# Performance work log

Hardware: AMD Instinct MI355X
Metric: run time of the kernel (lower is better)

Reference implementation:

```python
import jax, jax.numpy as jnp
import numpy as np

B = 2
L = 512                         # latent dim
NF = [64, 128, 256, 512, 512]   # _get_num_features(2*base_features=64, 64, max=512)


def _rn(key, shape, scale=1.0):
    return scale * jax.random.normal(key, shape, dtype=jnp.float32)


def _blur_up(x):
    """upfirdn2d: 2x upsample + FIR blur with resample_kernel [1,3,3,1], gain=factor**2."""
    k = jnp.array([1.0, 3.0, 3.0, 1.0], dtype=x.dtype)
    kk = jnp.outer(k, k)
    kk = kk / kk.sum() * 4.0  # gain = 2**2
    c = x.shape[-1]
    kern = jnp.broadcast_to(kk[:, :, None, None], (4, 4, 1, c))
    return jax.lax.conv_general_dilated(
        x, kern, (1, 1), ((2, 2), (2, 2)), lhs_dilation=(2, 2),
        dimension_numbers=('NHWC', 'HWIO', 'NHWC'), feature_group_count=c)


def _mod_conv(x, latent, w, b, sw, sb, demodulate):
    """StyleGAN2 modulated conv. x:(B,H,W,Cin), w:(kh,kw,Cin,Cout), style affine (L,Cin)."""
    s = latent @ sw + sb                             # (B,Cin) style
    ww = w[None] * s[:, None, None, :, None]         # (B,kh,kw,Cin,Cout)
    if demodulate:
        d = jax.lax.rsqrt(jnp.sum(ww * ww, axis=(1, 2, 3)) + 1e-8)  # (B,Cout)
        ww = ww * d[:, None, None, None, :]
    def per_sample(xi, wi):
        return jax.lax.conv_general_dilated(
            xi[None], wi, (1, 1), 'SAME',
            dimension_numbers=('NHWC', 'HWIO', 'NHWC'))[0]
    return jax.vmap(per_sample)(x, ww) + b


def _forward(latents, const, w0, b0, sw0, sb0, ns0, noise0, wr0, br0, swr0, sbr0,
             wu1, bu1, swu1, sbu1, wc1, bc1, swc1, sbc1, wr1, br1, swr1, sbr1,
             wu2, bu2, swu2, sbu2, wc2, bc2, swc2, sbc2, wr2, br2, swr2, sbr2,
             wu3, bu3, swu3, sbu3, wc3, bc3, swc3, sbc3, wr3, br3, swr3, sbr3,
             wu4, bu4, swu4, sbu4, wc4, bc4, swc4, sbc4, wr4, br4, swr4, sbr4):
    act = lambda t: jax.nn.leaky_relu(t, 0.01)
    b = latents.shape[0]
    lat = latents.reshape(b, 2, 5, latents.shape[-1])  # (B,2,n_levels,L)
    # first layer at 4x4: modulated conv + noise + leaky_relu (only layer with noise, per source)
    y = _mod_conv(jnp.tile(const[None], (b, 1, 1, 1)), lat[:, 0, 0], w0, b0, sw0, sb0, True)
    y = act(y + ns0 * noise0)
    rgb = act(_mod_conv(y, lat[:, 0, 1], wr0, br0, swr0, sbr0, False))
    ups = [(wu1, bu1, swu1, sbu1), (wu2, bu2, swu2, sbu2), (wu3, bu3, swu3, sbu3), (wu4, bu4, swu4, sbu4)]
    cvs = [(wc1, bc1, swc1, sbc1), (wc2, bc2, swc2, sbc2), (wc3, bc3, swc3, sbc3), (wc4, bc4, swc4, sbc4)]
    rgbs = [(wr1, br1, swr1, sbr1), (wr2, br2, swr2, sbr2), (wr3, br3, swr3, sbr3), (wr4, br4, swr4, sbr4)]
    for i in range(1, 5):
        wu, bu, swu, sbu = ups[i - 1]
        wc, bc, swc, sbc = cvs[i - 1]
        wr, br, swr, sbr = rgbs[i - 1]
        y = _mod_conv(_blur_up(y), lat[:, i - 1, 1], wu, bu, swu, sbu, True)
        # plain ModulatedConv2D 3x3 (no noise/activation in the source loop)
        y = _mod_conv(y, lat[:, i, 0], wc, bc, swc, sbc, True)
        # to_rgb (no demod) + skip accumulation of FIR-upsampled previous rgb
        rgb = act(_mod_conv(y, lat[:, i, 1], wr, br, swr, sbr, False)) + _blur_up(rgb)
    return rgb  # (B,64,64,3)


reference = _forward


def setup_inputs():
    key = jax.random.key(0)
    ks = iter(jax.random.split(key, 80))
    inp = {}
    inp['latents'] = _rn(next(ks), (B, 2 * 5, L))
    inp['const'] = _rn(next(ks), (4, 4, NF[-1]))
    def mod(pfx, kh, cin, cout):
        inp['w' + pfx] = _rn(next(ks), (kh, kh, cin, cout), (kh * kh * cin) ** -0.5)
        inp['b' + pfx] = jnp.zeros((cout,), jnp.float32)
        inp['sw' + pfx] = _rn(next(ks), (L, cin), L ** -0.5)
        inp['sb' + pfx] = jnp.ones((cin,), jnp.float32)
    mod('0', 3, NF[-1], NF[-1])
    inp['ns0'] = 0.1 * _rn(next(ks), (1, 1, 1, 1))
    inp['noise0'] = _rn(next(ks), (B, 4, 4, 1))
    mod('r0', 1, NF[-1], 3)
    cprev = NF[-1]
    for i in range(1, 5):
        c = NF[i]
        mod('u%d' % i, 3, cprev, c)
        mod('c%d' % i, 3, c, c)
        mod('r%d' % i, 1, c, 3)
        cprev = c
    return inp
```

## Files before the change

kernel.cpp:

```cpp
#include <hip/hip_runtime.h>

#define LEAKY(v) ((v) > 0.f ? (v) : 0.01f * (v))

typedef __attribute__((ext_vector_type(8))) short bf16x8;
typedef __attribute__((ext_vector_type(4))) short bf16x4;
typedef __attribute__((ext_vector_type(4))) float floatx4;

__device__ inline unsigned short f2bf(float f) {
  unsigned u = __float_as_uint(f);
  unsigned r = u + 0x7FFFu + ((u >> 16) & 1u);
  return (unsigned short)(r >> 16);
}

__device__ inline bf16x8 ld_frag8(const unsigned short* p) {
  bf16x4 lo = *(const bf16x4*)p;
  bf16x4 hi = *(const bf16x4*)(p + 4);
  return __builtin_shufflevector(lo, hi, 0, 1, 2, 3, 4, 5, 6, 7);
}

struct StyleDesc { const float* sw; const float* sb; int row; int cin; };
struct StyleArgs { StyleDesc d[14]; };
struct W2D { const float* w; int cinLog; int coutLog; int start; int w2off; };
struct W2Args { W2D d[9]; int total4; };
struct WTD { const float* src; unsigned short* dst; int cinLog; int coutLog; int start; };
struct WTArgs { WTD d[6]; int totalTiles; };

__device__ void style_body(int bid, const float* __restrict__ lat, const StyleArgs& A,
                           float* __restrict__ S)
{
  int chunk = bid & 1, b = (bid >> 1) & 1, sid = bid >> 2;
  StyleDesc d = A.d[sid];
  int ci = chunk * 256 + threadIdx.x;
  if (ci >= d.cin) return;
  const float* l = lat + (size_t)b * (10 * 512) + d.row * 512;
  float a0 = 0.f, a1 = 0.f, a2 = 0.f, a3 = 0.f, a4 = 0.f, a5 = 0.f, a6 = 0.f, a7 = 0.f;
  const float* wp = d.sw + ci;
  size_t st = d.cin;
  for (int k = 0; k < 512; k += 8) {
    a0 += l[k] * wp[0];
    a1 += l[k + 1] * wp[st];
    a2 += l[k + 2] * wp[2 * st];
    a3 += l[k + 3] * wp[3 * st];
    a4 += l[k + 4] * wp[4 * st];
    a5 += l[k + 5] * wp[5 * st];
    a6 += l[k + 6] * wp[6 * st];
    a7 += l[k + 7] * wp[7 * st];
    wp += 8 * st;
  }
  S[sid * 1024 + b * 512 + ci] = d.sb[ci] + ((a0 + a1) + (a2 + a3)) + ((a4 + a5) + (a6 + a7));
}

__device__ void w2_body(int idx, const W2Args& A, float* __restrict__ W2)
{
  if (idx >= A.total4) return;
  int c = 0;
  while (c < 8 && idx >= A.d[c + 1].start) c++;
  W2D d = A.d[c];
  int rel = idx - d.start;
  int co4Log = d.coutLog - 2;
  int ci = rel >> co4Log;
  int co = (rel & ((1 << co4Log) - 1)) << 2;
  size_t ktStride = (size_t)(1 << d.cinLog) << d.coutLog;
  const float* p = d.w + ((size_t)ci << d.coutLog) + co;
  float4 acc = {0.f, 0.f, 0.f, 0.f};
#pragma unroll
  for (int kt = 0; kt < 9; kt++) {
    float4 v = *(const float4*)(p + kt * ktStride);
    acc.x += v.x * v.x; acc.y += v.y * v.y; acc.z += v.z * v.z; acc.w += v.w * v.w;
  }
  *(float4*)(W2 + d.w2off + ((size_t)ci << d.coutLog) + co) = acc;
}

__device__ void wprep_tile_body(int tile, const WTArgs& A, unsigned short* __restrict__ tl)
{
  int c = 0;
  while (c < 5 && tile >= A.d[c + 1].start) c++;
  WTD d = A.d[c];
  int rel = tile - d.start;
  int coTiles = 1 << (d.coutLog - 6);
  int cig = rel / coTiles;
  int co0 = (rel - cig * coTiles) << 6;
  int cin = 1 << d.cinLog, cout = 1 << d.coutLog;
  int tid = threadIdx.x;
  for (int slot = tid; slot < 288 * 16; slot += 256) {
    int r = slot >> 4;
    int co4 = slot & 15;
    int kt = r >> 5, cisub = r & 31;
    const float* sp = d.src + ((size_t)(kt * cin + (cig << 5) + cisub) << d.coutLog) + co0 + co4 * 4;
    float4 v = *(const float4*)sp;
    int cb = co4 * 4;
    tl[(cb + 0) * 296 + r] = f2bf(v.x);
    tl[(cb + 1) * 296 + r] = f2bf(v.y);
    tl[(cb + 2) * 296 + r] = f2bf(v.z);
    tl[(cb + 3) * 296 + r] = f2bf(v.w);
  }
  __syncthreads();
  int Kp = cin * 9;
  for (int slot = tid; slot < 64 * 36; slot += 256) {
    int co = slot / 36, c8 = slot - (slot / 36) * 36;
    bf16x4 lo = *(const bf16x4*)(tl + co * 296 + c8 * 8);
    bf16x4 hi = *(const bf16x4*)(tl + co * 296 + c8 * 8 + 4);
    unsigned short* op = d.dst + (size_t)(co0 + co) * Kp + cig * 288 + c8 * 8;
    *(bf16x4*)op = lo;
    *(bf16x4*)(op + 4) = hi;
  }
}

__global__ __launch_bounds__(256) void prep_all_kernel(
    const float* __restrict__ lat, StyleArgs SA, W2Args WA, WTArgs TA,
    float* __restrict__ S, float* __restrict__ W2, int styleBlocks, int w2Blocks)
{
  __shared__ unsigned short tl[64 * 296];
  int bid = blockIdx.x;
  if (bid < styleBlocks) { style_body(bid, lat, SA, S); return; }
  bid -= styleBlocks;
  if (bid < w2Blocks) { w2_body(bid * 256 + threadIdx.x, WA, W2); return; }
  bid -= w2Blocks;
  if (bid < TA.totalTiles) wprep_tile_body(bid, TA, tl);
}

struct D2D { int w2off; int sid; int did; int cin; int cout; int start; };
struct D2Args { D2D d[9]; };

__global__ __launch_bounds__(256) void demod2_all_kernel(
    D2Args A, const float* __restrict__ W2, const float* __restrict__ S,
    float* __restrict__ Dout)
{
  __shared__ float red[256];
  int bid = blockIdx.x;
  int c = 0;
  while (c < 8 && bid >= A.d[c + 1].start) c++;
  D2D d = A.d[c];
  int rel = bid - d.start;
  int chunksPerB = d.cout >> 6;
  int b = rel / chunksPerB;
  int coc = rel - b * chunksPerB;
  int co = coc * 64 + (threadIdx.x & 63);
  int slice = threadIdx.x >> 6;
  const float* sv = S + d.sid * 1024 + b * 512;
  const float* wp = W2 + d.w2off + co;
  float a0 = 0.f, a1 = 0.f, a2 = 0.f, a3 = 0.f, a4 = 0.f, a5 = 0.f, a6 = 0.f, a7 = 0.f;
  for (int r = slice; r < d.cin; r += 32) {
    float s0 = sv[r];          a0 += s0 * s0 * wp[(size_t)r * d.cout];
    float s1 = sv[r + 4];      a1 += s1 * s1 * wp[(size_t)(r + 4) * d.cout];
    float s2 = sv[r + 8];      a2 += s2 * s2 * wp[(size_t)(r + 8) * d.cout];
    float s3 = sv[r + 12];     a3 += s3 * s3 * wp[(size_t)(r + 12) * d.cout];
    float s4 = sv[r + 16];     a4 += s4 * s4 * wp[(size_t)(r + 16) * d.cout];
    float s5 = sv[r + 20];     a5 += s5 * s5 * wp[(size_t)(r + 20) * d.cout];
    float s6 = sv[r + 24];     a6 += s6 * s6 * wp[(size_t)(r + 24) * d.cout];
    float s7 = sv[r + 28];     a7 += s7 * s7 * wp[(size_t)(r + 28) * d.cout];
  }
  red[threadIdx.x] = ((a0 + a1) + (a2 + a3)) + ((a4 + a5) + (a6 + a7));
  __syncthreads();
  if (threadIdx.x < 64) {
    float a = red[threadIdx.x] + red[threadIdx.x + 64] + red[threadIdx.x + 128] + red[threadIdx.x + 192];
    Dout[d.did * 1024 + b * 512 + co] = rsqrtf(a + 1e-8f);
  }
}

__device__ inline void blur_taps(int o, int* r0, int* r1, float* w0, float* w1)
{
  if ((o & 1) == 0) { *r0 = (o >> 1) - 1; *w0 = 1.f; *r1 = (o >> 1); *w1 = 3.f; }
  else              { *r0 = (o - 1) >> 1; *w0 = 3.f; *r1 = ((o - 1) >> 1) + 1; *w1 = 1.f; }
}

__global__ __launch_bounds__(256) void prep_up_kernel(
    const float* __restrict__ y, int Hc, int C,
    const float* __restrict__ s, unsigned short* __restrict__ out)
{
  int b = blockIdx.y;
  int W2 = Hc * 2;
  int pix = blockIdx.x;
  int oy = pix / W2, ox = pix - oy * W2;
  int ry0, ry1, rx0, rx1; float wy0, wy1, wx0, wx1;
  blur_taps(oy, &ry0, &ry1, &wy0, &wy1);
  blur_taps(ox, &rx0, &rx1, &wx0, &wx1);
  bool vy0 = (ry0 >= 0 && ry0 < Hc), vy1 = (ry1 >= 0 && ry1 < Hc);
  bool vx0 = (rx0 >= 0 && rx0 < Hc), vx1 = (rx1 >= 0 && rx1 < Hc);
  const float* base = y + (size_t)b * Hc * Hc * C;
  unsigned short* ob = out + (((size_t)b * W2 + oy) * W2 + ox) * C;
  const float* sv = s + b * 512;
  for (int c = threadIdx.x; c < C; c += 256) {
    float acc = 0.f;
    if (vy0) {
      const float* r = base + (size_t)(ry0 * Hc) * C;
      if (vx0) acc += wy0 * wx0 * r[(size_t)rx0 * C + c];
      if (vx1) acc += wy0 * wx1 * r[(size_t)rx1 * C + c];
    }
    if (vy1) {
      const float* r = base + (size_t)(ry1 * Hc) * C;
      if (vx0) acc += wy1 * wx0 * r[(size_t)rx0 * C + c];
      if (vx1) acc += wy1 * wx1 * r[(size_t)rx1 * C + c];
    }
    ob[c] = f2bf(acc * (1.f / 16.f) * sv[c]);
  }
}

__global__ __launch_bounds__(256) void mfma_conv_kernel(
    const unsigned short* __restrict__ xp, int H, int WLOG, int Cin, int Cout,
    const unsigned short* __restrict__ wT,
    const float* __restrict__ bias, const float* __restrict__ dmod,
    float* __restrict__ outF, unsigned short* __restrict__ outBf,
    const float* __restrict__ sNext)
{
  extern __shared__ unsigned short sm[];
  const int W = 1 << WLOG;
  const int Rt = 128 >> WLOG;
  const int PR = Rt + 2, PC = W + 2;
  const int patchU = PR * PC * 36;
  unsigned short* Bw = sm + patchU;

  const int tid = threadIdx.x;
  const int wave = tid >> 6;
  const int lane = tid & 63;
  const int q = lane >> 4;
  const int l15 = lane & 15;

  const int HW = H << WLOG;
  const int m0 = blockIdx.x << 7;
  const int b = m0 / HW;
  const int y0 = (m0 - b * HW) >> WLOG;
  const int co0 = blockIdx.y << 6;
  const int Kp = Cin * 9;
  const unsigned short* xb = xp + (size_t)b * HW * Cin;

  const int pSlots = PR * PC * 4;
  int pLds[5], pSrc[5];
#pragma unroll
  for (int i = 0; i < 5; i++) {
    int sidx = tid + i * 256;
    pLds[i] = -1; pSrc[i] = -1;
    if (sidx < pSlots) {
      int pidx = sidx >> 2, part = sidx & 3;
      int pr = pidx / PC, pc = pidx - pr * PC;
      int gy = y0 + pr - 1, gx = pc - 1;
      pLds[i] = pidx * 36 + part * 8;
      if ((unsigned)gy < (unsigned)H && (unsigned)gx < (unsigned)W)
        pSrc[i] = ((gy << WLOG) + gx) * Cin + part * 8;
    }
  }
  int bLds[9], bSrc[9];
#pragma unroll
  for (int i = 0; i < 9; i++) {
    int sidx = tid + i * 256;
    int n = sidx / 36, c16 = sidx - n * 36;
    bLds[i] = n * 292 + c16 * 8;
    bSrc[i] = (co0 + n) * Kp + c16 * 8;
  }

  floatx4 zero = {0.f, 0.f, 0.f, 0.f};
  floatx4 acc[2][4];
#pragma unroll
  for (int mi = 0; mi < 2; mi++)
#pragma unroll
    for (int s = 0; s < 4; s++) acc[mi][s] = zero;

  const int mA0 = wave * 32 + l15;
  const int mA1 = mA0 + 16;
  const int aBase0 = ((mA0 >> WLOG) * PC + (mA0 & (W - 1))) * 36 + q * 8;
  const int aBase1 = ((mA1 >> WLOG) * PC + (mA1 & (W - 1))) * 36 + q * 8;
  const int bBase = l15 * 292 + q * 8;

  const int nGroups = Cin >> 5;

  uint4 pv[5], bv[9];
  {
#pragma unroll
    for (int i = 0; i < 5; i++) {
      uint4 v = {0u, 0u, 0u, 0u};
      if (pLds[i] >= 0 && pSrc[i] >= 0) v = *(const uint4*)(xb + pSrc[i]);
      pv[i] = v;
    }
#pragma unroll
    for (int i = 0; i < 9; i++) bv[i] = *(const uint4*)(wT + bSrc[i]);
  }

  for (int g = 0; g < nGroups; g++) {
    __syncthreads();
#pragma unroll
    for (int i = 0; i < 5; i++) {
      if (pLds[i] >= 0) {
        uint2 lo = {pv[i].x, pv[i].y}, hi = {pv[i].z, pv[i].w};
        *(uint2*)(sm + pLds[i]) = lo;
        *(uint2*)(sm + pLds[i] + 4) = hi;
      }
    }
#pragma unroll
    for (int i = 0; i < 9; i++) {
      uint2 lo = {bv[i].x, bv[i].y}, hi = {bv[i].z, bv[i].w};
      *(uint2*)(Bw + bLds[i]) = lo;
      *(uint2*)(Bw + bLds[i] + 4) = hi;
    }
    __syncthreads();
    if (g + 1 < nGroups) {
      const int gci = (g + 1) << 5;
      const int gw = (g + 1) * 288;
#pragma unroll
      for (int i = 0; i < 5; i++) {
        uint4 v = {0u, 0u, 0u, 0u};
        if (pLds[i] >= 0 && pSrc[i] >= 0) v = *(const uint4*)(xb + pSrc[i] + gci);
        pv[i] = v;
      }
#pragma unroll
      for (int i = 0; i < 9; i++) bv[i] = *(const uint4*)(wT + bSrc[i] + gw);
    }
#pragma unroll
    for (int kt = 0; kt < 9; kt++) {
      const int ky = kt / 3, kx = kt - (kt / 3) * 3;
      const int ao = (ky * PC + kx) * 36;
      bf16x8 a0 = ld_frag8(sm + aBase0 + ao);
      bf16x8 a1 = ld_frag8(sm + aBase1 + ao);
      const int bo = bBase + kt * 32;
#pragma unroll
      for (int s = 0; s < 4; s++) {
        bf16x8 bb = ld_frag8(Bw + bo + s * (16 * 292));
        acc[0][s] = __builtin_amdgcn_mfma_f32_16x16x32_bf16(a0, bb, acc[0][s], 0, 0, 0);
        acc[1][s] = __builtin_amdgcn_mfma_f32_16x16x32_bf16(a1, bb, acc[1][s], 0, 0, 0);
      }
    }
  }

#pragma unroll
  for (int s = 0; s < 4; s++) {
    const int co = co0 + s * 16 + l15;
    const float dm = dmod[b * 512 + co];
    const float bv2 = bias[co];
    const float sn = sNext ? sNext[b * 512 + co] : 0.f;
#pragma unroll
    for (int mi = 0; mi < 2; mi++) {
#pragma unroll
      for (int r = 0; r < 4; r++) {
        const int mloc = wave * 32 + mi * 16 + q * 4 + r;
        const int py = y0 + (mloc >> WLOG);
        const int px = mloc & (W - 1);
        const size_t oidx = (((size_t)b * H + py) * W + px) * Cout + co;
        const float v = acc[mi][s][r] * dm + bv2;
        if (outF) outF[oidx] = v;
        if (outBf) outBf[oidx] = f2bf(v * sn);
      }
    }
  }
}

template<int PIX, int NCI4>
__global__ __launch_bounds__(256) void modconv_splitk_kernel(
    const float* __restrict__ x, size_t xBStride, int H, int W, int cinShift,
    int Cout,
    const float* __restrict__ w, const float* __restrict__ s,
    float* __restrict__ partial)
{
  constexpr int NCI = NCI4 * 4;
  constexpr int CLOG = (NCI == 16) ? 4 : (NCI == 32) ? 5 : 6;
  extern __shared__ float lds[];
  const int COLS = PIX + 2;
  const int tid = threadIdx.x;
  const int nthr = blockDim.x;
  const int b = blockIdx.y;
  const int z = blockIdx.z;
  const int ci0 = z << CLOG;
  const int wb = W / PIX;
  const int row = blockIdx.x / wb;
  const int x0 = (blockIdx.x % wb) * PIX;

  const float* xb = x + (size_t)b * xBStride;
  const float* sv = s + b * 512;

  const int tot = 3 * COLS << CLOG;
  for (int idx = tid; idx < tot; idx += nthr) {
    int cil = idx & (NCI - 1);
    int t = idx >> CLOG;
    int col = t % COLS;
    int ry = t / COLS;
    int gy = row + ry - 1;
    int gx = x0 + col - 1;
    float v = 0.f;
    if (gy >= 0 && gy < H && gx >= 0 && gx < W)
      v = xb[((size_t)(gy * W + gx) << cinShift) + ci0 + cil] * sv[ci0 + cil];
    lds[idx] = v;
  }
  __syncthreads();

  float acc0[PIX];
  float acc1[PIX];
#pragma unroll
  for (int p = 0; p < PIX; p++) { acc0[p] = 0.f; acc1[p] = 0.f; }
  const int co0 = tid;
  const int co1 = tid + nthr;
  const bool a0 = co0 < Cout;
  const bool a1 = co1 < Cout;
  const int d01 = nthr;

  const float4* ldsv = (const float4*)lds;
  constexpr int cin4Shift = CLOG - 2;

  for (int kt = 0; kt < 9; kt++) {
    int ky = kt / 3, kx = kt % 3;
    const float* wr = w + ((size_t)(kt << cinShift) + ci0) * Cout + co0;
#pragma unroll
    for (int c4 = 0; c4 < NCI4; c4++) {
      float wA0 = 0.f, wA1 = 0.f, wA2 = 0.f, wA3 = 0.f;
      float wB0 = 0.f, wB1 = 0.f, wB2 = 0.f, wB3 = 0.f;
      const float* wq = wr + (size_t)c4 * 4 * Cout;
      if (a0) { wA0 = wq[0]; }
      if (a1) { wB0 = wq[d01]; }
      if (a0) { wA1 = wq[Cout]; }
      if (a1) { wB1 = wq[Cout + d01]; }
      if (a0) { wA2 = wq[2 * Cout]; }
      if (a1) { wB2 = wq[2 * Cout + d01]; }
      if (a0) { wA3 = wq[3 * Cout]; }
      if (a1) { wB3 = wq[3 * Cout + d01]; }
#pragma unroll
      for (int p = 0; p < PIX; p++) {
        float4 v = ldsv[((ky * COLS + kx + p) << cin4Shift) + c4];
        acc0[p] += v.x * wA0; acc0[p] += v.y * wA1; acc0[p] += v.z * wA2; acc0[p] += v.w * wA3;
        acc1[p] += v.x * wB0; acc1[p] += v.y * wB1; acc1[p] += v.z * wB2; acc1[p] += v.w * wB3;
      }
    }
  }

  const int HW = H * W;
  float* pb = partial + ((size_t)(z * gridDim.y + b) * HW + row * W + x0) * Cout;
#pragma unroll
  for (int p = 0; p < PIX; p++) {
    if (a0) pb[(size_t)p * Cout + co0] = acc0[p];
    if (a1) pb[(size_t)p * Cout + co1] = acc1[p];
  }
}

__global__ __launch_bounds__(128) void modconv_splitk_blur_kernel(
    const float* __restrict__ y, const float* __restrict__ w,
    const float* __restrict__ s, float* __restrict__ partial)
{
  extern __shared__ float lds[];
  const int tid = threadIdx.x;
  const int b = blockIdx.y;
  const int z = blockIdx.z;
  const int ci0 = z << 4;
  const int row = blockIdx.x;

  const float* yb = y + (size_t)b * 16 * 512;
  const float* sv = s + b * 512;

  for (int idx = tid; idx < 480; idx += 128) {
    int cil = idx & 15;
    int t = idx >> 4;
    int col = t % 10;
    int ry = t / 10;
    int gy = row + ry - 1;
    int gx = col - 1;
    float v = 0.f;
    if ((unsigned)gy < 8u && (unsigned)gx < 8u) {
      int ry0, ry1, rx0, rx1; float wy0, wy1, wx0, wx1;
      blur_taps(gy, &ry0, &ry1, &wy0, &wy1);
      blur_taps(gx, &rx0, &rx1, &wx0, &wx1);
      bool vy0 = (ry0 >= 0 && ry0 < 4), vy1 = (ry1 >= 0 && ry1 < 4);
      bool vx0 = (rx0 >= 0 && rx0 < 4), vx1 = (rx1 >= 0 && rx1 < 4);
      int ci = ci0 + cil;
      float acc = 0.f;
      if (vy0 && vx0) acc += wy0 * wx0 * yb[((ry0 * 4 + rx0) << 9) + ci];
      if (vy0 && vx1) acc += wy0 * wx1 * yb[((ry0 * 4 + rx1) << 9) + ci];
      if (vy1 && vx0) acc += wy1 * wx0 * yb[((ry1 * 4 + rx0) << 9) + ci];
      if (vy1 && vx1) acc += wy1 * wx1 * yb[((ry1 * 4 + rx1) << 9) + ci];
      v = acc * (1.f / 16.f) * sv[ci];
    }
    lds[idx] = v;
  }
  __syncthreads();

  float acc0[8];
#pragma unroll
  for (int p = 0; p < 8; p++) acc0[p] = 0.f;
  const int co0 = tid;
  const float4* ldsv = (const float4*)lds;

  for (int kt = 0; kt < 9; kt++) {
    int ky = kt / 3, kx = kt % 3;
    const float* wr = w + ((size_t)(kt << 9) + ci0) * 128 + co0;
#pragma unroll
    for (int c4 = 0; c4 < 4; c4++) {
      const float* wq = wr + (size_t)c4 * 4 * 128;
      float wA0 = wq[0];
      float wA1 = wq[128];
      float wA2 = wq[256];
      float wA3 = wq[384];
#pragma unroll
      for (int p = 0; p < 8; p++) {
        float4 v = ldsv[((ky * 10 + kx + p) << 2) + c4];
        acc0[p] += v.x * wA0; acc0[p] += v.y * wA1; acc0[p] += v.z * wA2; acc0[p] += v.w * wA3;
      }
    }
  }

  float* pb = partial + ((size_t)(z * gridDim.y + b) * 64 + row * 8) * 128;
#pragma unroll
  for (int p = 0; p < 8; p++) pb[(size_t)p * 128 + co0] = acc0[p];
}

__global__ __launch_bounds__(256) void splitk_epi_kernel(
    const float* __restrict__ partial, int nz, int M, int Cout, int HW,
    const float* __restrict__ dmod, const float* __restrict__ bias,
    float* __restrict__ out)
{
  int idx = blockIdx.x * 256 + threadIdx.x;
  if (idx >= M * Cout) return;
  int m = idx / Cout;
  int co = idx - m * Cout;
  int b = m / HW;
  float acc = 0.f;
  for (int z = 0; z < nz; z++) acc += partial[(size_t)z * M * Cout + idx];
  out[idx] = acc * dmod[b * 512 + co] + bias[co];
}

__global__ void epirgb_kernel(
    const float* __restrict__ P, int nz, int HW, int Cout, int W,
    const float* __restrict__ dmod, const float* __restrict__ bias,
    const float* __restrict__ noise, const float* __restrict__ ns, int doAct,
    const float* __restrict__ sR, const float* __restrict__ wR, const float* __restrict__ bR,
    const float* __restrict__ prev,
    float* __restrict__ yout, float* __restrict__ rgbout)
{
  __shared__ float red[24];
  int b = blockIdx.x / HW;
  int pix = blockIdx.x - b * HW;
  int co = threadIdx.x;
  int m = b * HW + pix;
  float acc = 0.f;
  for (int z = 0; z < nz; z++) acc += P[((size_t)(z * 2 + b) * HW + pix) * Cout + co];
  float v = acc * dmod[b * 512 + co] + bias[co];
  if (noise) v += ns[0] * noise[m];
  if (doAct) v = LEAKY(v);
  yout[(size_t)m * Cout + co] = v;
  float t = v * sR[b * 512 + co];
  float r0 = t * wR[co * 3 + 0];
  float r1 = t * wR[co * 3 + 1];
  float r2 = t * wR[co * 3 + 2];
  for (int off = 32; off > 0; off >>= 1) {
    r0 += __shfl_down(r0, off);
    r1 += __shfl_down(r1, off);
    r2 += __shfl_down(r2, off);
  }
  int wv = threadIdx.x >> 6, lane = threadIdx.x & 63;
  if (lane == 0) { red[wv * 3 + 0] = r0; red[wv * 3 + 1] = r1; red[wv * 3 + 2] = r2; }
  __syncthreads();
  if (threadIdx.x == 0) {
    int nw = blockDim.x >> 6;
    float s0 = bR[0], s1 = bR[1], s2 = bR[2];
    for (int w = 0; w < nw; w++) { s0 += red[w * 3]; s1 += red[w * 3 + 1]; s2 += red[w * 3 + 2]; }
    s0 = LEAKY(s0); s1 = LEAKY(s1); s2 = LEAKY(s2);
    if (prev) {
      int oy = pix / W, ox = pix - (pix / W) * W;
      int Hp = W >> 1;
      int ry0, ry1, rx0, rx1; float wy0, wy1, wx0, wx1;
      blur_taps(oy, &ry0, &ry1, &wy0, &wy1);
      blur_taps(ox, &rx0, &rx1, &wx0, &wx1);
      bool vy0 = (ry0 >= 0 && ry0 < Hp), vy1 = (ry1 >= 0 && ry1 < Hp);
      bool vx0 = (rx0 >= 0 && rx0 < Hp), vx1 = (rx1 >= 0 && rx1 < Hp);
      const float* base = prev + (size_t)b * Hp * Hp * 3;
      float a0 = 0.f, a1 = 0.f, a2 = 0.f;
      if (vy0 && vx0) { const float* qq = base + (size_t)(ry0 * Hp + rx0) * 3; float wg = wy0 * wx0; a0 += wg * qq[0]; a1 += wg * qq[1]; a2 += wg * qq[2]; }
      if (vy0 && vx1) { const float* qq = base + (size_t)(ry0 * Hp + rx1) * 3; float wg = wy0 * wx1; a0 += wg * qq[0]; a1 += wg * qq[1]; a2 += wg * qq[2]; }
      if (vy1 && vx0) { const float* qq = base + (size_t)(ry1 * Hp + rx0) * 3; float wg = wy1 * wx0; a0 += wg * qq[0]; a1 += wg * qq[1]; a2 += wg * qq[2]; }
      if (vy1 && vx1) { const float* qq = base + (size_t)(ry1 * Hp + rx1) * 3; float wg = wy1 * wx1; a0 += wg * qq[0]; a1 += wg * qq[1]; a2 += wg * qq[2]; }
      s0 += a0 * (1.f / 16.f); s1 += a1 * (1.f / 16.f); s2 += a2 * (1.f / 16.f);
    }
    rgbout[(size_t)m * 3 + 0] = s0;
    rgbout[(size_t)m * 3 + 1] = s1;
    rgbout[(size_t)m * 3 + 2] = s2;
  }
}

__global__ __launch_bounds__(64) void rgb_kernel(
    const float* __restrict__ y, int H, int W, int Cin,
    const float* __restrict__ w, const float* __restrict__ bias,
    const float* __restrict__ s, const float* __restrict__ prev,
    float* __restrict__ out)
{
  int b = blockIdx.y;
  int pix = blockIdx.x;
  int oy = pix / W, ox = pix % W;
  const float* xp = y + (((size_t)b * H + oy) * W + ox) * Cin;
  const float* sv = s + b * 512;
  float p0 = 0.f, p1 = 0.f, p2 = 0.f;
  for (int ci = threadIdx.x; ci < Cin; ci += 64) {
    float v = xp[ci] * sv[ci];
    p0 += v * w[ci * 3 + 0];
    p1 += v * w[ci * 3 + 1];
    p2 += v * w[ci * 3 + 2];
  }
  for (int off = 32; off > 0; off >>= 1) {
    p0 += __shfl_down(p0, off);
    p1 += __shfl_down(p1, off);
    p2 += __shfl_down(p2, off);
  }
  if (threadIdx.x == 0) {
    float r0 = p0 + bias[0], r1 = p1 + bias[1], r2 = p2 + bias[2];
    float sk0 = 0.f, sk1 = 0.f, sk2 = 0.f;
    if (prev) {
      int Hp = H >> 1, Wp = W >> 1;
      int ry0, ry1, rx0, rx1; float wy0, wy1, wx0, wx1;
      blur_taps(oy, &ry0, &ry1, &wy0, &wy1);
      blur_taps(ox, &rx0, &rx1, &wx0, &wx1);
      bool vy0 = (ry0 >= 0 && ry0 < Hp), vy1 = (ry1 >= 0 && ry1 < Hp);
      bool vx0 = (rx0 >= 0 && rx0 < Wp), vx1 = (rx1 >= 0 && rx1 < Wp);
      const float* base = prev + (size_t)b * Hp * Wp * 3;
      float a0 = 0.f, a1 = 0.f, a2 = 0.f;
      if (vy0 && vx0) { const float* qq = base + (size_t)(ry0 * Wp + rx0) * 3; float wg = wy0 * wx0; a0 += wg * qq[0]; a1 += wg * qq[1]; a2 += wg * qq[2]; }
      if (vy0 && vx1) { const float* qq = base + (size_t)(ry0 * Wp + rx1) * 3; float wg = wy0 * wx1; a0 += wg * qq[0]; a1 += wg * qq[1]; a2 += wg * qq[2]; }
      if (vy1 && vx0) { const float* qq = base + (size_t)(ry1 * Wp + rx0) * 3; float wg = wy1 * wx0; a0 += wg * qq[0]; a1 += wg * qq[1]; a2 += wg * qq[2]; }
      if (vy1 && vx1) { const float* qq = base + (size_t)(ry1 * Wp + rx1) * 3; float wg = wy1 * wx1; a0 += wg * qq[0]; a1 += wg * qq[1]; a2 += wg * qq[2]; }
      sk0 = a0 * (1.f / 16.f); sk1 = a1 * (1.f / 16.f); sk2 = a2 * (1.f / 16.f);
    }
    float* ob = out + (((size_t)b * H + oy) * W + ox) * 3;
    ob[0] = LEAKY(r0) + sk0;
    ob[1] = LEAKY(r1) + sk1;
    ob[2] = LEAKY(r2) + sk2;
  }
}

extern "C" void kernel_launch(void* const* d_in, const int* in_sizes, int n_in,
                              void* d_out, int out_size, void* d_ws, size_t ws_size,
                              hipStream_t stream)
{
  auto F = [&](int k) { return (const float*)d_in[k]; };
  const float* latents = F(0);
  const float* cnst = F(1);
  const float* w0 = F(2);  const float* b0 = F(3);  const float* sw0 = F(4);  const float* sb0 = F(5);
  const float* ns0 = F(6); const float* noise0 = F(7);
  const float* wr0 = F(8); const float* br0 = F(9); const float* swr0 = F(10); const float* sbr0 = F(11);
  const float *wu[4], *bu[4], *swu[4], *sbu[4];
  const float *wc[4], *bc[4], *swc[4], *sbc[4];
  const float *wr[4], *br_[4], *swr[4], *sbr[4];
  int k = 12;
  for (int l = 0; l < 4; l++) {
    wu[l] = F(k++); bu[l] = F(k++); swu[l] = F(k++); sbu[l] = F(k++);
    wc[l] = F(k++); bc[l] = F(k++); swc[l] = F(k++); sbc[l] = F(k++);
    wr[l] = F(k++); br_[l] = F(k++); swr[l] = F(k++); sbr[l] = F(k++);
  }

  float* ws = (float*)d_ws;
  float* S = ws;
  float* D = S + 14 * 1024;
  float* W2 = D + 9 * 1024;
  float* bufA = W2 + 1359872;
  float* bufB = bufA + 2 * 64 * 64 * 512;
  float* rgbA = bufB + 2 * 64 * 64 * 512;
  float* rgbB = rgbA + 2 * 64 * 64 * 3;
  float* P = rgbB + 2 * 64 * 64 * 3;
  unsigned short* u16 = (unsigned short*)(P + 524288);
  unsigned short* xprepA = u16;
  unsigned short* xprepB = xprepA + 2 * 64 * 64 * 512;
  unsigned short* wT[6];
  {
    unsigned short* p = xprepB + 2 * 64 * 64 * 512;
    int wsz[6] = {9 * 128 * 256, 9 * 256 * 256, 9 * 256 * 512, 9 * 512 * 512, 9 * 512 * 512, 9 * 512 * 512};
    for (int i = 0; i < 6; i++) { wT[i] = p; p += wsz[i]; }
  }

  const int B = 2;
  const int NFa[5] = {64, 128, 256, 512, 512};
  int cprev0[4] = {512, 128, 256, 512};
  int rowu[4] = {1, 6, 6, 6};

  const float* cw[9]  = {w0, wu[0], wc[0], wu[1], wc[1], wu[2], wc[2], wu[3], wc[3]};
  int cinL[9]  = {9, 9, 7, 7, 8, 8, 9, 9, 9};
  int coutL[9] = {9, 7, 7, 8, 8, 9, 9, 9, 9};
  int sidOf[9] = {0, 2, 3, 5, 6, 8, 9, 11, 12};
  int didOf[9] = {0, 1, 2, 3, 4, 5, 6, 7, 8};

  int w2off[9];
  {
    StyleArgs SA;
    SA.d[0] = {sw0, sb0, 0, 512};
    SA.d[1] = {swr0, sbr0, 1, 512};
    for (int l = 0; l < 4; l++) {
      int c = NFa[l + 1];
      SA.d[2 + l * 3] = {swu[l], sbu[l], rowu[l], cprev0[l]};
      SA.d[3 + l * 3] = {swc[l], sbc[l], 5, c};
      SA.d[4 + l * 3] = {swr[l], sbr[l], 6, c};
    }
    W2Args WA2;
    int w2start = 0, off = 0;
    for (int i = 0; i < 9; i++) {
      w2off[i] = off;
      WA2.d[i] = {cw[i], cinL[i], coutL[i], w2start, off};
      int elems = 1 << (cinL[i] + coutL[i]);
      w2start += elems >> 2;
      off += elems;
    }
    WA2.total4 = w2start;
    WTArgs TA;
    {
      const float* srcs[6] = {wu[1], wc[1], wu[2], wc[2], wu[3], wc[3]};
      int cinLg[6] = {7, 8, 8, 9, 9, 9};
      int coutLg[6] = {8, 8, 9, 9, 9, 9};
      int start = 0;
      for (int i = 0; i < 6; i++) {
        TA.d[i] = {srcs[i], wT[i], cinLg[i], coutLg[i], start};
        start += (1 << (cinLg[i] - 5)) * (1 << (coutLg[i] - 6));
      }
      TA.totalTiles = start;
    }
    int styleBlocks = 56;
    int w2Blocks = (WA2.total4 + 255) / 256;
    prep_all_kernel<<<dim3(styleBlocks + w2Blocks + TA.totalTiles), 256, 0, stream>>>(
        latents, SA, WA2, TA, S, W2, styleBlocks, w2Blocks);
  }

  {
    D2Args DA;
    int start = 0;
    for (int i = 0; i < 9; i++) {
      int cout = 1 << coutL[i];
      DA.d[i] = {w2off[i], sidOf[i], didOf[i], 1 << cinL[i], cout, start};
      start += B * (cout >> 6);
    }
    demod2_all_kernel<<<dim3(start), 256, 0, stream>>>(DA, W2, S, D);
  }

  modconv_splitk_kernel<4, 4><<<dim3(4, B, 32), 256, (size_t)3 * 6 * 16 * 4, stream>>>(
      cnst, 0, 4, 4, 9, 512, w0, S, P);
  epirgb_kernel<<<dim3(B * 16), 512, 0, stream>>>(
      P, 32, 16, 512, 4, D, b0, noise0, ns0, 1,
      S + 1024, wr0, br0, nullptr, bufA, rgbA);

  modconv_splitk_blur_kernel<<<dim3(8, B, 32), 128, (size_t)480 * 4, stream>>>(
      bufA, wu[0], S + 2 * 1024, P);
  splitk_epi_kernel<<<dim3((128 * 128 + 255) / 256), 256, 0, stream>>>(
      P, 32, 128, 128, 64, D + 1 * 1024, bu[0], bufA);
  modconv_splitk_kernel<8, 4><<<dim3(8, B, 8), 128, (size_t)3 * 10 * 16 * 4, stream>>>(
      bufA, (size_t)64 * 128, 8, 8, 7, 128, wc[0], S + 3 * 1024, P);
  epirgb_kernel<<<dim3(B * 64), 128, 0, stream>>>(
      P, 8, 64, 128, 8, D + 2 * 1024, bc[0], nullptr, nullptr, 0,
      S + 4 * 1024, wr[0], br_[0], rgbA, bufB, rgbB);

  float* ybuf[4] = {bufB, bufA, bufB, bufA};
  float* rgbp = rgbB;
  const float* ysrc = bufB;
  int Hc = 8;
  for (int l = 1; l < 4; l++) {
    int c = NFa[l + 1];
    int cp = cprev0[l];
    int H2 = Hc * 2;
    int WLOG = (H2 == 16) ? 4 : (H2 == 32) ? 5 : 6;
    int wi = (l - 1) * 2;
    prep_up_kernel<<<dim3(H2 * H2, B), 256, 0, stream>>>(
        ysrc, Hc, cp, S + (2 + l * 3) * 1024, xprepA);
    {
      int PRu = (128 >> WLOG) + 2, PCu = H2 + 2;
      size_t lds = (size_t)(PRu * PCu * 36 + 64 * 292) * 2;
      mfma_conv_kernel<<<dim3((B * H2 * H2) / 128, c >> 6), 256, lds, stream>>>(
          xprepA, H2, WLOG, cp, c, wT[wi], bu[l], D + (1 + l * 2) * 1024,
          nullptr, xprepB, S + (3 + l * 3) * 1024);
    }
    float* yo = ybuf[l];
    {
      int PRu = (128 >> WLOG) + 2, PCu = H2 + 2;
      size_t lds = (size_t)(PRu * PCu * 36 + 64 * 292) * 2;
      mfma_conv_kernel<<<dim3((B * H2 * H2) / 128, c >> 6), 256, lds, stream>>>(
          xprepB, H2, WLOG, c, c, wT[wi + 1], bc[l], D + (2 + l * 2) * 1024,
          yo, nullptr, nullptr);
    }
    float* rout = (l == 3) ? (float*)d_out : ((rgbp == rgbA) ? rgbB : rgbA);
    rgb_kernel<<<dim3(H2 * H2, B), 64, 0, stream>>>(
        yo, H2, H2, c, wr[l], br_[l], S + (4 + l * 3) * 1024, rgbp, rout);
    rgbp = (rout == rgbA) ? rgbA : rgbB;
    ysrc = yo;
    Hc = H2;
  }
  (void)in_sizes; (void)n_in; (void)out_size; (void)ws_size;
}
```

Measured before the change: 553.5 us.

## Switch conv kernel to 32x32x16 MFMA with 2-wave blocks and 16-byte LDS

Rewrites the implicit-GEMM conv kernel to use 32x32x16 bf16 MFMA tiles, two per wave in each dimension, with 128-thread blocks instead of 256 and 16x16x32 tiles. LDS rows are padded to 40/296 elements so fragments load as single 16-byte vectors. The register prefetch of the next channel group is removed, and global loads now go straight to LDS. This aims to raise MFMA efficiency and cut LDS instruction count, but it gives up the load/compute overlap and halves the waves per block.

Result: slower. 973.0 us (+75.8%).

```diff
diff --git a/kernel.cpp b/kernel.cpp
--- a/kernel.cpp
+++ b/kernel.cpp
@@ -3,19 +3,12 @@
 #define LEAKY(v) ((v) > 0.f ? (v) : 0.01f * (v))
 
 typedef __attribute__((ext_vector_type(8))) short bf16x8;
-typedef __attribute__((ext_vector_type(4))) short bf16x4;
-typedef __attribute__((ext_vector_type(4))) float floatx4;
+typedef __attribute__((ext_vector_type(16))) float floatx16;
 
 __device__ inline unsigned short f2bf(float f) {
   unsigned u = __float_as_uint(f);
   unsigned r = u + 0x7FFFu + ((u >> 16) & 1u);
   return (unsigned short)(r >> 16);
-}
-
-__device__ inline bf16x8 ld_frag8(const unsigned short* p) {
-  bf16x4 lo = *(const bf16x4*)p;
-  bf16x4 hi = *(const bf16x4*)(p + 4);
-  return __builtin_shufflevector(lo, hi, 0, 1, 2, 3, 4, 5, 6, 7);
 }
 
 struct StyleDesc { const float* sw; const float* sb; int row; int cin; };
@@ -80,7 +73,7 @@
   int coTiles = 1 << (d.coutLog - 6);
   int cig = rel / coTiles;
   int co0 = (rel - cig * coTiles) << 6;
-  int cin = 1 << d.cinLog, cout = 1 << d.coutLog;
+  int cin = 1 << d.cinLog;
   int tid = threadIdx.x;
   for (int slot = tid; slot < 288 * 16; slot += 256) {
     int r = slot >> 4;
@@ -98,11 +91,11 @@
   int Kp = cin * 9;
   for (int slot = tid; slot < 64 * 36; slot += 256) {
     int co = slot / 36, c8 = slot - (slot / 36) * 36;
-    bf16x4 lo = *(const bf16x4*)(tl + co * 296 + c8 * 8);
-    bf16x4 hi = *(const bf16x4*)(tl + co * 296 + c8 * 8 + 4);
+    uint2 lo = *(const uint2*)(tl + co * 296 + c8 * 8);
+    uint2 hi = *(const uint2*)(tl + co * 296 + c8 * 8 + 4);
     unsigned short* op = d.dst + (size_t)(co0 + co) * Kp + cig * 288 + c8 * 8;
-    *(bf16x4*)op = lo;
-    *(bf16x4*)(op + 4) = hi;
+    *(uint2*)op = lo;
+    *(uint2*)(op + 4) = hi;
   }
 }
 
@@ -196,7 +189,7 @@
   }
 }
 
-__global__ __launch_bounds__(256) void mfma_conv_kernel(
+__global__ __launch_bounds__(128) void mfma_conv_kernel(
     const unsigned short* __restrict__ xp, int H, int WLOG, int Cin, int Cout,
     const unsigned short* __restrict__ wT,
     const float* __restrict__ bias, const float* __restrict__ dmod,
@@ -207,14 +200,15 @@
   const int W = 1 << WLOG;
   const int Rt = 128 >> WLOG;
   const int PR = Rt + 2, PC = W + 2;
-  const int patchU = PR * PC * 36;
+  const int patchU = PR * PC * 40;
   unsigned short* Bw = sm + patchU;
 
   const int tid = threadIdx.x;
   const int wave = tid >> 6;
   const int lane = tid & 63;
-  const int q = lane >> 4;
-  const int l15 = lane & 15;
+  const int l31 = lane & 31;
+  const int half = lane >> 5;
+  const int koff = half * 8;
 
   const int HW = H << WLOG;
   const int m0 = blockIdx.x << 7;
@@ -225,116 +219,101 @@
   const unsigned short* xb = xp + (size_t)b * HW * Cin;
 
   const int pSlots = PR * PC * 4;
-  int pLds[5], pSrc[5];
-#pragma unroll
-  for (int i = 0; i < 5; i++) {
-    int sidx = tid + i * 256;
+  int pLds[9], pSrc[9];
+#pragma unroll
+  for (int i = 0; i < 9; i++) {
+    int sidx = tid + i * 128;
     pLds[i] = -1; pSrc[i] = -1;
     if (sidx < pSlots) {
       int pidx = sidx >> 2, part = sidx & 3;
       int pr = pidx / PC, pc = pidx - pr * PC;
       int gy = y0 + pr - 1, gx = pc - 1;
-      pLds[i] = pidx * 36 + part * 8;
+      pLds[i] = pidx * 40 + part * 8;
       if ((unsigned)gy < (unsigned)H && (unsigned)gx < (unsigned)W)
         pSrc[i] = ((gy << WLOG) + gx) * Cin + part * 8;
     }
   }
-  int bLds[9], bSrc[9];
-#pragma unroll
-  for (int i = 0; i < 9; i++) {
-    int sidx = tid + i * 256;
+  int bLds[18], bSrc[18];
+#pragma unroll
+  for (int i = 0; i < 18; i++) {
+    int sidx = tid + i * 128;
     int n = sidx / 36, c16 = sidx - n * 36;
-    bLds[i] = n * 292 + c16 * 8;
+    bLds[i] = n * 296 + c16 * 8;
     bSrc[i] = (co0 + n) * Kp + c16 * 8;
   }
 
-  floatx4 zero = {0.f, 0.f, 0.f, 0.f};
-  floatx4 acc[2][4];
+  floatx16 acc[2][2];
 #pragma unroll
   for (int mi = 0; mi < 2; mi++)
 #pragma unroll
-    for (int s = 0; s < 4; s++) acc[mi][s] = zero;
-
-  const int mA0 = wave * 32 + l15;
-  const int mA1 = mA0 + 16;
-  const int aBase0 = ((mA0 >> WLOG) * PC + (mA0 & (W - 1))) * 36 + q * 8;
-  const int aBase1 = ((mA1 >> WLOG) * PC + (mA1 & (W - 1))) * 36 + q * 8;
-  const int bBase = l15 * 292 + q * 8;
+    for (int ni = 0; ni < 2; ni++)
+#pragma unroll
+      for (int r = 0; r < 16; r++) acc[mi][ni][r] = 0.f;
+
+  int aBase[2];
+#pragma unroll
+  for (int mi = 0; mi < 2; mi++) {
+    int pix = wave * 64 + mi * 32 + l31;
+    aBase[mi] = ((pix >> WLOG) * PC + (pix & (W - 1))) * 40 + koff;
+  }
+  int bBase[2];
+#pragma unroll
+  for (int ni = 0; ni < 2; ni++)
+    bBase[ni] = (ni * 32 + l31) * 296 + koff;
 
   const int nGroups = Cin >> 5;
-
-  uint4 pv[5], bv[9];
-  {
-#pragma unroll
-    for (int i = 0; i < 5; i++) {
-      uint4 v = {0u, 0u, 0u, 0u};
-      if (pLds[i] >= 0 && pSrc[i] >= 0) v = *(const uint4*)(xb + pSrc[i]);
-      pv[i] = v;
-    }
-#pragma unroll
-    for (int i = 0; i < 9; i++) bv[i] = *(const uint4*)(wT + bSrc[i]);
-  }
-
   for (int g = 0; g < nGroups; g++) {
     __syncthreads();
-#pragma unroll
-    for (int i = 0; i < 5; i++) {
-      if (pLds[i] >= 0) {
-        uint2 lo = {pv[i].x, pv[i].y}, hi = {pv[i].z, pv[i].w};
-        *(uint2*)(sm + pLds[i]) = lo;
-        *(uint2*)(sm + pLds[i] + 4) = hi;
+    {
+      const int gci = g << 5;
+#pragma unroll
+      for (int i = 0; i < 9; i++) {
+        if (pLds[i] >= 0) {
+          uint4 v = {0u, 0u, 0u, 0u};
+          if (pSrc[i] >= 0) v = *(const uint4*)(xb + pSrc[i] + gci);
+          *(uint4*)(sm + pLds[i]) = v;
+        }
       }
-    }
-#pragma unroll
-    for (int i = 0; i < 9; i++) {
-      uint2 lo = {bv[i].x, bv[i].y}, hi = {bv[i].z, bv[i].w};
-      *(uint2*)(Bw + bLds[i]) = lo;
-      *(uint2*)(Bw + bLds[i] + 4) = hi;
+      const int gw = g * 288;
+#pragma unroll
+      for (int i = 0; i < 18; i++)
+        *(uint4*)(Bw + bLds[i]) = *(const uint4*)(wT + bSrc[i] + gw);
     }
     __syncthreads();
-    if (g + 1 < nGroups) {
-      const int gci = (g + 1) << 5;
-      const int gw = (g + 1) * 288;
-#pragma unroll
-      for (int i = 0; i < 5; i++) {
-        uint4 v = {0u, 0u, 0u, 0u};
-        if (pLds[i] >= 0 && pSrc[i] >= 0) v = *(const uint4*)(xb + pSrc[i] + gci);
-        pv[i] = v;
-      }
-#pragma unroll
-      for (int i = 0; i < 9; i++) bv[i] = *(const uint4*)(wT + bSrc[i] + gw);
-    }
 #pragma unroll
     for (int kt = 0; kt < 9; kt++) {
       const int ky = kt / 3, kx = kt - (kt / 3) * 3;
-      const int ao = (ky * PC + kx) * 36;
-      bf16x8 a0 = ld_frag8(sm + aBase0 + ao);
-      bf16x8 a1 = ld_frag8(sm + aBase1 + ao);
-      const int bo = bBase + kt * 32;
-#pragma unroll
-      for (int s = 0; s < 4; s++) {
-        bf16x8 bb = ld_frag8(Bw + bo + s * (16 * 292));
-        acc[0][s] = __builtin_amdgcn_mfma_f32_16x16x32_bf16(a0, bb, acc[0][s], 0, 0, 0);
-        acc[1][s] = __builtin_amdgcn_mfma_f32_16x16x32_bf16(a1, bb, acc[1][s], 0, 0, 0);
+      const int ao = (ky * PC + kx) * 40;
+      const int bo = kt * 32;
+#pragma unroll
+      for (int s = 0; s < 2; s++) {
+        bf16x8 a0 = *(const bf16x8*)(sm + aBase[0] + ao + s * 16);
+        bf16x8 a1 = *(const bf16x8*)(sm + aBase[1] + ao + s * 16);
+        bf16x8 b0 = *(const bf16x8*)(Bw + bBase[0] + bo + s * 16);
+        bf16x8 b1 = *(const bf16x8*)(Bw + bBase[1] + bo + s * 16);
+        acc[0][0] = __builtin_amdgcn_mfma_f32_32x32x16_bf16(a0, b0, acc[0][0], 0, 0, 0);
+        acc[0][1] = __builtin_amdgcn_mfma_f32_32x32x16_bf16(a0, b1, acc[0][1], 0, 0, 0);
+        acc[1][0] = __builtin_amdgcn_mfma_f32_32x32x16_bf16(a1, b0, acc[1][0], 0, 0, 0);
+        acc[1][1] = __builtin_amdgcn_mfma_f32_32x32x16_bf16(a1, b1, acc[1][1], 0, 0, 0);
       }
     }
   }
 
 #pragma unroll
-  for (int s = 0; s < 4; s++) {
-    const int co = co0 + s * 16 + l15;
+  for (int ni = 0; ni < 2; ni++) {
+    const int co = co0 + ni * 32 + l31;
     const float dm = dmod[b * 512 + co];
-    const float bv2 = bias[co];
+    const float bv = bias[co];
     const float sn = sNext ? sNext[b * 512 + co] : 0.f;
 #pragma unroll
     for (int mi = 0; mi < 2; mi++) {
 #pragma unroll
-      for (int r = 0; r < 4; r++) {
-        const int mloc = wave * 32 + mi * 16 + q * 4 + r;
+      for (int r = 0; r < 16; r++) {
+        const int mloc = wave * 64 + mi * 32 + (r & 3) + 8 * (r >> 2) + 4 * half;
         const int py = y0 + (mloc >> WLOG);
         const int px = mloc & (W - 1);
         const size_t oidx = (((size_t)b * H + py) * W + px) * Cout + co;
-        const float v = acc[mi][s][r] * dm + bv2;
+        const float v = acc[mi][ni][r] * dm + bv;
         if (outF) outF[oidx] = v;
         if (outBf) outBf[oidx] = f2bf(v * sn);
       }
@@ -747,16 +726,16 @@
         ysrc, Hc, cp, S + (2 + l * 3) * 1024, xprepA);
     {
       int PRu = (128 >> WLOG) + 2, PCu = H2 + 2;
-      size_t lds = (size_t)(PRu * PCu * 36 + 64 * 292) * 2;
-      mfma_conv_kernel<<<dim3((B * H2 * H2) / 128, c >> 6), 256, lds, stream>>>(
+      size_t lds = (size_t)(PRu * PCu * 40 + 64 * 296) * 2;
+      mfma_conv_kernel<<<dim3((B * H2 * H2) / 128, c >> 6), 128, lds, stream>>>(
           xprepA, H2, WLOG, cp, c, wT[wi], bu[l], D + (1 + l * 2) * 1024,
           nullptr, xprepB, S + (3 + l * 3) * 1024);
     }
     float* yo = ybuf[l];
     {
       int PRu = (128 >> WLOG) + 2, PCu = H2 + 2;
-      size_t lds = (size_t)(PRu * PCu * 36 + 64 * 292) * 2;
-      mfma_conv_kernel<<<dim3((B * H2 * H2) / 128, c >> 6), 256, lds, stream>>>(
+      size_t lds = (size_t)(PRu * PCu * 40 + 64 * 296) * 2;
+      mfma_conv_kernel<<<dim3((B * H2 * H2) / 128, c >> 6), 128, lds, stream>>>(
           xprepB, H2, WLOG, c, c, wT[wi + 1], bc[l], D + (2 + l * 2) * 1024,
           yo, nullptr, nullptr);
     }
```
